# Optimization experiments

Hardware: AMD Instinct MI355X
Metric: run time of the kernel (lower is better)

The kernel has to match this reference:

```python
import jax, jax.numpy as jnp
import numpy as np

B, S, D = 4, 2048, 1024


def setup_inputs() -> dict:
    key = jax.random.key(0)
    kx, kq, kk, kv, km = jax.random.split(key, 5)
    bound = 1.0 / np.sqrt(D)  # torch Linear default init range
    X = jax.random.normal(kx, (B, S, D), dtype=jnp.float32)
    Wq = jax.random.uniform(kq, (D, D), jnp.float32, -bound, bound)
    Wk = jax.random.uniform(kk, (D, D), jnp.float32, -bound, bound)
    Wv = jax.random.uniform(kv, (D, D), jnp.float32, -bound, bound)
    masks = jax.random.randint(km, (B, S), 0, 2, dtype=jnp.int32)
    return {"X": X, "masks": masks, "Wq": Wq, "Wk": Wk, "Wv": Wv}


def reference(X, masks, Wq, Wk, Wv):
    n = X.shape[1]
    # mask construction: True where masked (padding OR future position)
    lookahead = jnp.triu(jnp.ones((n, n), dtype=bool), k=1)          # [S,S]
    pad = ~(masks.astype(bool))[:, None, :]                           # [B,1,S] -> key-side padding
    m = (pad | lookahead[None]).astype(X.dtype)                       # [B,S,S]

    # Linear layers (torch: y = x @ W.T)
    Q = jnp.einsum('bsd,ed->bse', X, Wq)
    K = jnp.einsum('bsd,ed->bse', X, Wk)
    V = jnp.einsum('bsd,ed->bse', X, Wv)

    # cosine-normalized attention scores, multiplied (not added) by the mask
    Qn = Q / jnp.linalg.norm(Q, axis=-1, keepdims=True)
    Kn = K / jnp.linalg.norm(K, axis=-1, keepdims=True)
    scores = jnp.einsum('bqd,bkd->bqk', Qn, Kn) * m                   # [B,S,S]
    return jnp.einsum('bqk,bkd->bqd', scores, V)
```

## Files before the change

### kernel.cpp

```cpp
#include <hip/hip_runtime.h>
#include <hip/hip_bf16.h>

#define B_ 4
#define S_ 2048
#define D_ 1024
#define MTOT (B_ * S_)

typedef __attribute__((ext_vector_type(8))) short bf16x8;
typedef __attribute__((ext_vector_type(4))) float f32x4;

__device__ __forceinline__ unsigned short f2bf(float f) {
  union { float f; unsigned int u; } v; v.f = f;
  unsigned int r = v.u + 0x7FFFu + ((v.u >> 16) & 1u);
  return (unsigned short)(r >> 16);
}
__device__ __forceinline__ float bf2f(unsigned short u) {
  union { unsigned int u; float f; } v; v.u = ((unsigned int)u) << 16;
  return v.f;
}

__global__ __launch_bounds__(256) void cvt_all(const float* __restrict__ X,
                                               const float* __restrict__ Wq,
                                               const float* __restrict__ Wk,
                                               const float* __restrict__ Wv,
                                               unsigned short* __restrict__ Xb,
                                               unsigned short* __restrict__ Wqkv) {
  long i = (long)blockIdx.x * 256 + threadIdx.x;
  const float* src;
  unsigned short* dst;
  long off;
  if (i < 2097152L) {
    src = X; dst = Xb; off = i;
  } else {
    long j = i - 2097152L;
    int w = (int)(j >> 18);
    off = j & 262143L;
    src = (w == 0) ? Wq : (w == 1) ? Wk : Wv;
    dst = Wqkv + (long)w * 1048576L;
  }
  float4 v = ((const float4*)src)[off];
  ushort4 o;
  o.x = f2bf(v.x); o.y = f2bf(v.y); o.z = f2bf(v.z); o.w = f2bf(v.w);
  ((ushort4*)dst)[off] = o;
}

__global__ __launch_bounds__(256) void norms_bf16(const unsigned short* __restrict__ QKraw,
                                                  float* __restrict__ rq,
                                                  float* __restrict__ rk) {
  int row = blockIdx.x;
  int half = blockIdx.y;
  int tid = threadIdx.x;
  const unsigned short* src = QKraw + (long)half * MTOT * D_ + (long)row * D_;
  ushort4 u = *(const ushort4*)(src + tid * 4);
  float x0 = bf2f(u.x), x1 = bf2f(u.y), x2 = bf2f(u.z), x3 = bf2f(u.w);
  float ss = x0 * x0 + x1 * x1 + x2 * x2 + x3 * x3;
#pragma unroll
  for (int o = 1; o < 64; o <<= 1) ss += __shfl_xor(ss, o);
  __shared__ float wsum[4];
  if ((tid & 63) == 0) wsum[tid >> 6] = ss;
  __syncthreads();
  if (tid == 0) {
    float r = rsqrtf(wsum[0] + wsum[1] + wsum[2] + wsum[3]);
    (half ? rk : rq)[row] = r;
  }
}


#define GLDS16(g, l)                                                                   \
  __builtin_amdgcn_global_load_lds((const __attribute__((address_space(1))) void*)(g), \
                                   (__attribute__((address_space(3))) void*)(l), 16, 0, 0)

template <int EPI, int BN>
__global__ __launch_bounds__(256, 4) void gemm_k64(const unsigned short* __restrict__ A,
                                                   const unsigned short* __restrict__ B,
                                                   void* __restrict__ Cv, int N, int K,
                                                   long strideA, long strideB, long strideC,
                                                   const int* __restrict__ masks,
                                                   const float* __restrict__ rqp,
                                                   const float* __restrict__ rkp) {
  constexpr int NBF = BN / 32;
  __shared__ __align__(16) short lA[128 * 64];
  __shared__ __align__(16) short lB[BN * 64];
  __shared__ float srq[128], srk[128];
  __shared__ int smask[128];

  const int z = blockIdx.z;
  const unsigned short* Ab = A + (long)z * strideA;
  const unsigned short* Bb = B + (long)z * strideB;
  const int t = threadIdx.x;
  const int lane = t & 63, w = t >> 6;
  const int wr = w >> 1, wc = w & 1;
  const int fr = lane & 15, fq = lane >> 4;
  const int brow = blockIdx.x * 128, bcol = blockIdx.y * BN;
  const long K2 = (long)K * 2;

  if constexpr (EPI == 2) {
    if (t < 128) {
      smask[t] = masks[(long)z * S_ + bcol + t];
      srk[t] = rkp[(long)z * S_ + bcol + t];
    } else {
      srq[t - 128] = rqp[(long)z * S_ + brow + (t - 128)];
    }
  }

  const int srow = t >> 3;
  const int sslot = ((t & 7) ^ (srow & 7)) << 4;
  const char* gAs = (const char*)Ab + (long)(brow + srow) * K2 + sslot;
  const char* gBs = (const char*)Bb + (long)(bcol + srow) * K2 + sslot;
  const long jstr = (long)32 * K2;
  char* lAd = (char*)&lA[0] + t * 16;
  char* lBd = (char*)&lB[0] + t * 16;

#define STAGE()                                               \
  do {                                                        \
    _Pragma("unroll") for (int j = 0; j < 4; ++j)             \
        GLDS16(gAs + j * jstr, lAd + j * 4096);               \
    _Pragma("unroll") for (int j = 0; j < NBF; ++j)           \
        GLDS16(gBs + j * jstr, lBd + j * 4096);               \
    gAs += 128;                                               \
    gBs += 128;                                               \
  } while (0)

  f32x4 acc[4][NBF];
#pragma unroll
  for (int m = 0; m < 4; m++)
#pragma unroll
    for (int n = 0; n < NBF; n++) acc[m][n] = (f32x4){0.f, 0.f, 0.f, 0.f};

  int cbyte[2];
#pragma unroll
  for (int ks = 0; ks < 2; ++ks) cbyte[ks] = (((ks << 2) | fq) ^ (fr & 7)) << 4;
  const int arow0 = (wr * 64 + fr) << 7;
  const int brow0 = (wc * (BN / 2) + fr) << 7;

  const int NT = K / 64;
  for (int kt = 0; kt < NT; ++kt) {
    STAGE();
    __syncthreads();
#pragma unroll
    for (int ks = 0; ks < 2; ++ks) {
      bf16x8 af[4], bv[NBF];
#pragma unroll
      for (int m = 0; m < 4; m++)
        af[m] = *(const bf16x8*)((const char*)&lA[0] + arow0 + (m << 11) + cbyte[ks]);
#pragma unroll
      for (int n = 0; n < NBF; n++)
        bv[n] = *(const bf16x8*)((const char*)&lB[0] + brow0 + (n << 11) + cbyte[ks]);
#pragma unroll
      for (int m = 0; m < 4; m++)
#pragma unroll
        for (int n = 0; n < NBF; n++)
          acc[m][n] = __builtin_amdgcn_mfma_f32_16x16x32_bf16(af[m], bv[n], acc[m][n], 0, 0, 0);
    }
    if (kt + 1 < NT) __syncthreads();
  }
#undef STAGE

  long cbase = (long)z * strideC;
#pragma unroll
  for (int m = 0; m < 4; m++) {
#pragma unroll
    for (int n = 0; n < NBF; n++) {
#pragma unroll
      for (int r = 0; r < 4; r++) {
        int lr = wr * 64 + m * 16 + fq * 4 + r;
        int lc = wc * (BN / 2) + n * 16 + fr;
        int grow = brow + lr;
        int gcol = bcol + lc;
        float v = acc[m][n][r];
        if constexpr (EPI == 0) {
          ((float*)Cv)[cbase + (long)grow * N + gcol] = v;
        } else if constexpr (EPI == 1) {
          unsigned short* base = (unsigned short*)Cv;
          int seg = gcol >> 10, c = gcol & 1023;
          if (seg == 0) {
            base[(long)grow * D_ + c] = f2bf(v);
          } else if (seg == 1) {
            base[(long)MTOT * D_ + (long)grow * D_ + c] = f2bf(v);
          } else {
            int b = grow >> 11, s = grow & (S_ - 1);
            base[(long)2 * MTOT * D_ + (long)b * D_ * S_ + (long)c * S_ + s] = f2bf(v);
          }
        } else {
          bool keep = (gcol > grow) || (smask[lc] == 0);
          float sv = v * srq[lr] * srk[lc];
          ((unsigned short*)Cv)[cbase + (long)grow * N + gcol] = keep ? f2bf(sv) : (unsigned short)0;
        }
      }
    }
  }
}

extern "C" void kernel_launch(void* const* d_in, const int* in_sizes, int n_in, void* d_out,
                              int out_size, void* d_ws, size_t ws_size, hipStream_t stream) {
  (void)in_sizes; (void)n_in; (void)out_size; (void)ws_size;
  const float* X = (const float*)d_in[0];
  const int* masks = (const int*)d_in[1];
  const float* Wq = (const float*)d_in[2];
  const float* Wk = (const float*)d_in[3];
  const float* Wv = (const float*)d_in[4];
  float* out = (float*)d_out;

  char* ws = (char*)d_ws;
  unsigned short* Xb = (unsigned short*)ws;     ws += (long)MTOT * D_ * 2;
  unsigned short* Wqkv = (unsigned short*)ws;   ws += (long)3 * D_ * D_ * 2;
  unsigned short* QKVraw = (unsigned short*)ws; ws += (long)3 * MTOT * D_ * 2;
  float* rq = (float*)ws;                       ws += (long)MTOT * 4;
  float* rk = (float*)ws;                       ws += (long)MTOT * 4;
  unsigned short* Sm = (unsigned short*)ws;     ws += (long)B_ * S_ * S_ * 2;
  unsigned short* Qraw = QKVraw;
  unsigned short* Kraw = QKVraw + (long)MTOT * D_;
  unsigned short* Vt = QKVraw + (long)2 * MTOT * D_;

  cvt_all<<<11264, 256, 0, stream>>>(X, Wq, Wk, Wv, Xb, Wqkv);

  gemm_k64<1, 128><<<dim3(MTOT / 128, 3 * D_ / 128, 1), 256, 0, stream>>>(
      Xb, Wqkv, QKVraw, 3 * D_, D_, 0, 0, 0, nullptr, nullptr, nullptr);
  norms_bf16<<<dim3(MTOT, 2), 256, 0, stream>>>(QKVraw, rq, rk);
  gemm_k64<2, 128><<<dim3(S_ / 128, S_ / 128, B_), 256, 0, stream>>>(
      Qraw, Kraw, Sm, S_, D_, (long)S_ * D_, (long)S_ * D_, (long)S_ * S_, masks, rq, rk);
  gemm_k64<0, 64><<<dim3(S_ / 128, D_ / 64, B_), 256, 0, stream>>>(
      Sm, Vt, out, D_, S_, (long)S_ * S_, (long)D_ * S_, (long)S_ * D_, nullptr, nullptr, nullptr);
}
```

Before: 164.3 us.

## Double-buffer LDS tiles in GEMM to overlap global loads with MFMA

```diff
diff --git a/kernel.cpp b/kernel.cpp
--- a/kernel.cpp
+++ b/kernel.cpp
@@ -71,16 +71,18 @@
                                    (__attribute__((address_space(3))) void*)(l), 16, 0, 0)
 
 template <int EPI, int BN>
-__global__ __launch_bounds__(256, 4) void gemm_k64(const unsigned short* __restrict__ A,
-                                                   const unsigned short* __restrict__ B,
-                                                   void* __restrict__ Cv, int N, int K,
-                                                   long strideA, long strideB, long strideC,
-                                                   const int* __restrict__ masks,
-                                                   const float* __restrict__ rqp,
-                                                   const float* __restrict__ rkp) {
+__global__ __launch_bounds__(256, 2) void gemm_db(const unsigned short* __restrict__ A,
+                                                  const unsigned short* __restrict__ B,
+                                                  void* __restrict__ Cv, int N, int K,
+                                                  long strideA, long strideB, long strideC,
+                                                  const int* __restrict__ masks,
+                                                  const float* __restrict__ rqp,
+                                                  const float* __restrict__ rkp) {
   constexpr int NBF = BN / 32;
-  __shared__ __align__(16) short lA[128 * 64];
-  __shared__ __align__(16) short lB[BN * 64];
+  constexpr int ABUF = 128 * 64 * 2;
+  constexpr int BBUF = BN * 64 * 2;
+  __shared__ __align__(16) short lA[2][128 * 64];
+  __shared__ __align__(16) short lB[2][BN * 64];
   __shared__ float srq[128], srk[128];
   __shared__ int smask[128];
 
@@ -108,15 +110,17 @@
   const char* gAs = (const char*)Ab + (long)(brow + srow) * K2 + sslot;
   const char* gBs = (const char*)Bb + (long)(bcol + srow) * K2 + sslot;
   const long jstr = (long)32 * K2;
-  char* lAd = (char*)&lA[0] + t * 16;
-  char* lBd = (char*)&lB[0] + t * 16;
-
-#define STAGE()                                               \
+  char* lAd = (char*)&lA[0][0] + t * 16;
+  char* lBd = (char*)&lB[0][0] + t * 16;
+
+#define STAGE(buf)                                            \
   do {                                                        \
+    char* lad_ = lAd + (buf) * ABUF;                          \
+    char* lbd_ = lBd + (buf) * BBUF;                          \
     _Pragma("unroll") for (int j = 0; j < 4; ++j)             \
-        GLDS16(gAs + j * jstr, lAd + j * 4096);               \
+        GLDS16(gAs + j * jstr, lad_ + j * 4096);              \
     _Pragma("unroll") for (int j = 0; j < NBF; ++j)           \
-        GLDS16(gBs + j * jstr, lBd + j * 4096);               \
+        GLDS16(gBs + j * jstr, lbd_ + j * 4096);              \
     gAs += 128;                                               \
     gBs += 128;                                               \
   } while (0)
@@ -134,25 +138,30 @@
   const int brow0 = (wc * (BN / 2) + fr) << 7;
 
   const int NT = K / 64;
+  STAGE(0);
+  __syncthreads();
+
   for (int kt = 0; kt < NT; ++kt) {
-    STAGE();
-    __syncthreads();
+    const int cur = kt & 1;
+    if (kt + 1 < NT) STAGE(cur ^ 1);
+    const char* pa = (const char*)&lA[0][0] + cur * ABUF + arow0;
+    const char* pb = (const char*)&lB[0][0] + cur * BBUF + brow0;
 #pragma unroll
     for (int ks = 0; ks < 2; ++ks) {
       bf16x8 af[4], bv[NBF];
 #pragma unroll
       for (int m = 0; m < 4; m++)
-        af[m] = *(const bf16x8*)((const char*)&lA[0] + arow0 + (m << 11) + cbyte[ks]);
+        af[m] = *(const bf16x8*)(pa + (m << 11) + cbyte[ks]);
 #pragma unroll
       for (int n = 0; n < NBF; n++)
-        bv[n] = *(const bf16x8*)((const char*)&lB[0] + brow0 + (n << 11) + cbyte[ks]);
+        bv[n] = *(const bf16x8*)(pb + (n << 11) + cbyte[ks]);
 #pragma unroll
       for (int m = 0; m < 4; m++)
 #pragma unroll
         for (int n = 0; n < NBF; n++)
           acc[m][n] = __builtin_amdgcn_mfma_f32_16x16x32_bf16(af[m], bv[n], acc[m][n], 0, 0, 0);
     }
-    if (kt + 1 < NT) __syncthreads();
+    __syncthreads();
   }
 #undef STAGE
 
@@ -214,11 +223,11 @@
 
   cvt_all<<<11264, 256, 0, stream>>>(X, Wq, Wk, Wv, Xb, Wqkv);
 
-  gemm_k64<1, 128><<<dim3(MTOT / 128, 3 * D_ / 128, 1), 256, 0, stream>>>(
+  gemm_db<1, 128><<<dim3(MTOT / 128, 3 * D_ / 128, 1), 256, 0, stream>>>(
       Xb, Wqkv, QKVraw, 3 * D_, D_, 0, 0, 0, nullptr, nullptr, nullptr);
   norms_bf16<<<dim3(MTOT, 2), 256, 0, stream>>>(QKVraw, rq, rk);
-  gemm_k64<2, 128><<<dim3(S_ / 128, S_ / 128, B_), 256, 0, stream>>>(
+  gemm_db<2, 128><<<dim3(S_ / 128, S_ / 128, B_), 256, 0, stream>>>(
       Qraw, Kraw, Sm, S_, D_, (long)S_ * D_, (long)S_ * D_, (long)S_ * S_, masks, rq, rk);
-  gemm_k64<0, 64><<<dim3(S_ / 128, D_ / 64, B_), 256, 0, stream>>>(
+  gemm_db<0, 64><<<dim3(S_ / 128, D_ / 64, B_), 256, 0, stream>>>(
       Sm, Vt, out, D_, S_, (long)S_ * S_, (long)D_ * S_, (long)S_ * D_, nullptr, nullptr, nullptr);
 }
```

New measurement: 203.7 us. +24.0%, slower.
